# Optimization experiments

Measured on AMD Instinct MI355X. Metric: run time of the kernel, lower is better.

Reference implementation:

```python
import jax, jax.numpy as jnp
import numpy as np

N = 100000       # nodes
E = 1600000      # edges (before self loops)
D = 128          # emb_dim
L = 5            # num_layer
NBOND = 62       # num_bond_type
NNODE = 2159     # num_node_type + 2
BN_EPS = 1e-5


def setup_inputs() -> dict:
    key = jax.random.key(0)
    ks = jax.random.split(key, 8)
    x = jax.random.randint(ks[0], (N, 1), 0, NNODE)
    edge_index = jax.random.randint(ks[1], (2, E), 0, N)
    edge_attr = jax.random.randint(ks[2], (E, 1), 0, NBOND)
    x_emb = jax.random.normal(ks[3], (NNODE, D), dtype=jnp.float32) * 0.02
    lin_w = jax.random.normal(ks[4], (L, D, D), dtype=jnp.float32) * (1.0 / np.sqrt(D))
    lin_b = jnp.zeros((L, D), jnp.float32)
    edge_tab = jax.random.normal(ks[5], (L, NBOND, D), dtype=jnp.float32) * 0.02
    bn_gamma = jnp.ones((L, D), jnp.float32)
    bn_beta = jnp.zeros((L, D), jnp.float32)
    return {"x": x, "edge_index": edge_index, "edge_attr": edge_attr,
            "x_emb": x_emb, "lin_w": lin_w, "lin_b": lin_b,
            "edge_tab": edge_tab, "bn_gamma": bn_gamma, "bn_beta": bn_beta}


def reference(x, edge_index, edge_attr, x_emb, lin_w, lin_b, edge_tab, bn_gamma, bn_beta):
    # node embedding lookup: x_embedding(x[:, 0])
    h = x_emb[x[:, 0]]                                  # [N, D]

    # add self loops (same for every layer in the torch code)
    loop = jnp.arange(N)
    src = jnp.concatenate([edge_index[0], loop])        # [E+N] = j (source)
    dst = jnp.concatenate([edge_index[1], loop])        # [E+N] = i (target)
    eids = jnp.concatenate([edge_attr[:, 0], jnp.zeros((N,), edge_attr.dtype)])

    # GCN symmetric norm: deg from row (=src), deg_inv_sqrt[row]*deg_inv_sqrt[col]
    deg = jax.ops.segment_sum(jnp.ones(src.shape, h.dtype), src, num_segments=N)
    dinv = jnp.where(deg > 0, jax.lax.rsqrt(deg), jnp.zeros_like(deg))
    norm = (dinv[src] * dinv[dst])[:, None]             # [E+N, 1]

    for l in range(L):
        # linear transform of nodes
        hl = h @ lin_w[l].T + lin_b[l]                  # [N, D]
        # message: norm * (x_j + edge_embedding), gather from source nodes
        msg = norm * (hl[src] + edge_tab[l][eids])      # [E+N, D]
        # aggr='add': scatter_add into target nodes
        agg = jax.ops.segment_sum(msg, dst, num_segments=N)  # [N, D]
        # BatchNorm1d (training-mode batch statistics, biased variance)
        mean = agg.mean(axis=0)
        var = jnp.mean((agg - mean) ** 2, axis=0)
        h = (agg - mean) * jax.lax.rsqrt(var + BN_EPS) * bn_gamma[l] + bn_beta[l]
        if l < L - 1:
            h = jax.nn.relu(h)
        # dropout with drop_ratio=0 is identity
    # JK == 'last'
    return h
```

## Files before the change

### kernel.cpp

```cpp
#include <hip/hip_runtime.h>

#define NN 100000
#define NE 1600000
#define NT (NE + NN)
#define DD 128
#define NL 5
#define NB 62
#define BN_EPS 1e-5f
#define NBUCK 391
#define PSUMNB 6250

typedef unsigned short ushort_t;
typedef unsigned int uint_t;
typedef short bf8 __attribute__((ext_vector_type(8)));
typedef float f32x4 __attribute__((ext_vector_type(4)));

static __device__ __forceinline__ float4 ld4(const float* p) { return *(const float4*)p; }

static __device__ __forceinline__ float bfhi(uint_t u) {
    uint_t x = u & 0xFFFF0000u;
    return __builtin_bit_cast(float, x);
}
static __device__ __forceinline__ float bflo(uint_t u) {
    uint_t x = u << 16;
    return __builtin_bit_cast(float, x);
}
static __device__ __forceinline__ ushort_t f2bf(float f) {
    uint_t u = __builtin_bit_cast(uint_t, f);
    u += 0x7FFFu + ((u >> 16) & 1u);
    return (ushort_t)(u >> 16);
}


__global__ void k_init(int* gbh_d, int* gbh_s, float* scale, float* shift,
                       int* row_ptr) {
    int i = blockIdx.x * 256 + threadIdx.x;
    if (i < NBUCK) { gbh_d[i] = 0; gbh_s[i] = 0; }
    if (i < DD) { scale[i] = 1.f; shift[i] = 0.f; }
    if (i == 0) row_ptr[NN] = NT;
}

__global__ void k_cvt(const float* __restrict__ src, ushort_t* __restrict__ dst,
                      int total) {
    int i = blockIdx.x * 256 + threadIdx.x;
    if (i < total) dst[i] = f2bf(src[i]);
}

__global__ __launch_bounds__(256) void k_binhist(const int* __restrict__ ei,
                                                 int* __restrict__ gbh_d,
                                                 int* __restrict__ gbh_s) {
    __shared__ int hd[NBUCK], hs[NBUCK];
    int tid = threadIdx.x;
    for (int b = tid; b < NBUCK; b += 256) { hd[b] = 0; hs[b] = 0; }
    __syncthreads();
    for (int idx = blockIdx.x * 256 + tid; idx < NT; idx += gridDim.x * 256) {
        int d = (idx < NE) ? ei[NE + idx] : idx - NE;
        atomicAdd(&hd[d >> 8], 1);
        if (idx < NE) atomicAdd(&hs[ei[idx] >> 8], 1);
    }
    __syncthreads();
    for (int b = tid; b < NBUCK; b += 256) {
        if (hd[b]) atomicAdd(&gbh_d[b], hd[b]);
        if (hs[b]) atomicAdd(&gbh_s[b], hs[b]);
    }
}

__global__ void k_scan391(const int* __restrict__ gbh_d, const int* __restrict__ gbh_s,
                          int* __restrict__ bb_d, int* __restrict__ cur_d,
                          int* __restrict__ bb_s, int* __restrict__ cur_s) {
    __shared__ int s[512];
    const int* g = blockIdx.x ? gbh_s : gbh_d;
    int* bb = blockIdx.x ? bb_s : bb_d;
    int* cur = blockIdx.x ? cur_s : cur_d;
    int t = threadIdx.x;
    int v = (t < NBUCK) ? g[t] : 0;
    s[t] = v;
    __syncthreads();
    for (int off = 1; off < 512; off <<= 1) {
        int val = (t >= off) ? s[t - off] : 0;
        __syncthreads();
        s[t] += val;
        __syncthreads();
    }
    if (t < NBUCK) { int e = s[t] - v; bb[t] = e; cur[t] = e; }
    if (t == 511) bb[NBUCK] = s[511];
}

#define CHUNK 4096
__global__ __launch_bounds__(256) void k_scat_dst(const int* __restrict__ ei,
                                                  const int* __restrict__ ea,
                                                  int* __restrict__ gcur,
                                                  uint_t* __restrict__ rec) {
    __shared__ int lh[NBUCK];
    __shared__ int lbase[NBUCK];
    int tid = threadIdx.x;
    for (int b = tid; b < NBUCK; b += 256) lh[b] = 0;
    __syncthreads();
    int base = blockIdx.x * CHUNK;
    uint_t r[16];
    int bk[16];
#pragma unroll
    for (int k = 0; k < 16; ++k) {
        int idx = base + tid + k * 256;
        bk[k] = -1;
        if (idx < NT) {
            int s, d, eid;
            if (idx < NE) { s = ei[idx]; d = ei[NE + idx]; eid = ea[idx]; }
            else          { s = d = idx - NE; eid = 0; }
            bk[k] = d >> 8;
            r[k] = (uint_t)s | ((uint_t)eid << 17) | ((uint_t)(d & 255) << 24);
            atomicAdd(&lh[bk[k]], 1);
        }
    }
    __syncthreads();
    for (int b = tid; b < NBUCK; b += 256)
        if (lh[b]) lbase[b] = atomicAdd(&gcur[b], lh[b]);
    __syncthreads();
    for (int b = tid; b < NBUCK; b += 256) lh[b] = 0;
    __syncthreads();
#pragma unroll
    for (int k = 0; k < 16; ++k) {
        if (bk[k] >= 0) {
            int rk = atomicAdd(&lh[bk[k]], 1);
            rec[lbase[bk[k]] + rk] = r[k];
        }
    }
}

__global__ __launch_bounds__(256) void k_scat_src(const int* __restrict__ ei,
                                                  int* __restrict__ gcur,
                                                  int* __restrict__ rec) {
    __shared__ int lh[NBUCK];
    __shared__ int lbase[NBUCK];
    int tid = threadIdx.x;
    for (int b = tid; b < NBUCK; b += 256) lh[b] = 0;
    __syncthreads();
    int base = blockIdx.x * CHUNK;
    int r[16];
    int bk[16];
#pragma unroll
    for (int k = 0; k < 16; ++k) {
        int idx = base + tid + k * 256;
        bk[k] = -1;
        if (idx < NE) {
            r[k] = ei[idx];
            bk[k] = r[k] >> 8;
            atomicAdd(&lh[bk[k]], 1);
        }
    }
    __syncthreads();
    for (int b = tid; b < NBUCK; b += 256)
        if (lh[b]) lbase[b] = atomicAdd(&gcur[b], lh[b]);
    __syncthreads();
    for (int b = tid; b < NBUCK; b += 256) lh[b] = 0;
    __syncthreads();
#pragma unroll
    for (int k = 0; k < 16; ++k) {
        if (bk[k] >= 0) {
            int rk = atomicAdd(&lh[bk[k]], 1);
            rec[lbase[bk[k]] + rk] = r[k];
        }
    }
}

__global__ __launch_bounds__(256) void k_srcfin(const int* __restrict__ rec,
                                                const int* __restrict__ bb,
                                                float* __restrict__ dinv) {
    __shared__ int h[256];
    int tid = threadIdx.x;
    h[tid] = 0;
    __syncthreads();
    int lo = bb[blockIdx.x], hi = bb[blockIdx.x + 1];
    for (int i = lo + tid; i < hi; i += 256) atomicAdd(&h[rec[i] & 255], 1);
    __syncthreads();
    int v = blockIdx.x * 256 + tid;
    if (v < NN) dinv[v] = rsqrtf((float)(h[tid] + 1));
}

__global__ __launch_bounds__(256) void k_dstfin(const uint_t* __restrict__ rec,
                                                const int* __restrict__ bb,
                                                const float* __restrict__ dinv,
                                                int* __restrict__ row_ptr,
                                                int* __restrict__ s_pack,
                                                float* __restrict__ s_norm) {
    __shared__ int h[256], sc[256], rpE[256];
    int tid = threadIdx.x;
    h[tid] = 0;
    __syncthreads();
    int lo = bb[blockIdx.x], hi = bb[blockIdx.x + 1];
    for (int i = lo + tid; i < hi; i += 256) atomicAdd(&h[(rec[i] >> 24) & 255], 1);
    __syncthreads();
    sc[tid] = h[tid];
    __syncthreads();
    for (int off = 1; off < 256; off <<= 1) {
        int val = (tid >= off) ? sc[tid - off] : 0;
        __syncthreads();
        sc[tid] += val;
        __syncthreads();
    }
    rpE[tid] = sc[tid] - h[tid];
    int v = blockIdx.x * 256 + tid;
    if (v < NN) row_ptr[v] = lo + rpE[tid];
    h[tid] = 0;
    __syncthreads();
    for (int i = lo + tid; i < hi; i += 256) {
        uint_t u = rec[i];
        int dl = (u >> 24) & 255;
        int rk = atomicAdd(&h[dl], 1);
        int slot = lo + rpE[dl] + rk;
        int s = u & 0x1FFFF;
        int e = (u >> 17) & 0x3F;
        s_pack[slot] = s | (e << 20);
        s_norm[slot] = dinv[s] * dinv[(blockIdx.x << 8) + dl];
    }
}

__global__ void k_h0b(const int* __restrict__ x, const float* __restrict__ emb,
                      ushort_t* __restrict__ Xb, int n) {
    int v = blockIdx.x * 16 + (threadIdx.x >> 4);
    if (v >= n) return;
    int c8 = (threadIdx.x & 15) * 8;
    const float* src = &emb[x[v] * DD + c8];
    uint_t pk[4];
#pragma unroll
    for (int j = 0; j < 4; ++j)
        pk[j] = (uint_t)f2bf(src[2 * j]) | ((uint_t)f2bf(src[2 * j + 1]) << 16);
    *(uint4*)&Xb[(size_t)v * DD + c8] = make_uint4(pk[0], pk[1], pk[2], pk[3]);
}


__global__ __launch_bounds__(256, 2) void k_gemm(const ushort_t* __restrict__ Xb,
                                                 const ushort_t* __restrict__ Wb,
                                                 const float* __restrict__ bias,
                                                 const float* __restrict__ scale,
                                                 const float* __restrict__ shift,
                                                 ushort_t* __restrict__ C,
                                                 int n, int relu) {
    __shared__ ushort_t As[128 * DD];
    __shared__ ushort_t Bs[128 * DD];
    const int tid = threadIdx.x;
    const int r0 = blockIdx.x * 128;
    const int rl = tid >> 4;
    const int kg = tid & 15;

    float sc[8], sh[8];
    *(float4*)&sc[0] = ld4(&scale[kg * 8]);
    *(float4*)&sc[4] = ld4(&scale[kg * 8 + 4]);
    *(float4*)&sh[0] = ld4(&shift[kg * 8]);
    *(float4*)&sh[4] = ld4(&shift[kg * 8 + 4]);

#pragma unroll
    for (int it = 0; it < 8; ++it) {
        int row = rl + it * 16;
        int grow = r0 + row;
        uint4 v = make_uint4(0, 0, 0, 0);
        if (grow < n) v = *(const uint4*)&Xb[(size_t)grow * DD + kg * 8];
        uint_t pk[4];
        const uint_t* pv = (const uint_t*)&v;
#pragma unroll
        for (int j = 0; j < 4; ++j) {
            float lo = fmaf(bflo(pv[j]), sc[2 * j], sh[2 * j]);
            float hi = fmaf(bfhi(pv[j]), sc[2 * j + 1], sh[2 * j + 1]);
            if (relu) { lo = fmaxf(lo, 0.f); hi = fmaxf(hi, 0.f); }
            pk[j] = (uint_t)f2bf(lo) | ((uint_t)f2bf(hi) << 16);
        }
        *(uint4*)&As[row * DD + (kg ^ (row & 7)) * 8] = make_uint4(pk[0], pk[1], pk[2], pk[3]);
        uint4 wv = *(const uint4*)&Wb[row * DD + kg * 8];
        *(uint4*)&Bs[row * DD + (kg ^ (row & 7)) * 8] = wv;
    }
    __syncthreads();

    const int w = tid >> 6;
    const int lane = tid & 63;
    const int lr = lane & 15;
    const int lg = lane >> 4;

    f32x4 acc[2][8];
#pragma unroll
    for (int rf = 0; rf < 2; ++rf)
#pragma unroll
        for (int cf = 0; cf < 8; ++cf)
#pragma unroll
            for (int r = 0; r < 4; ++r) acc[rf][cf][r] = 0.f;

#pragma unroll
    for (int ks = 0; ks < 4; ++ks) {
        int kgg = ks * 4 + lg;
        bf8 a0, a1;
        {
            int row = w * 32 + lr;
            a0 = *(bf8*)&As[row * DD + (kgg ^ (row & 7)) * 8];
            row += 16;
            a1 = *(bf8*)&As[row * DD + (kgg ^ (row & 7)) * 8];
        }
#pragma unroll
        for (int cf = 0; cf < 8; ++cf) {
            int col = cf * 16 + lr;
            bf8 b = *(bf8*)&Bs[col * DD + (kgg ^ (col & 7)) * 8];
            acc[0][cf] = __builtin_amdgcn_mfma_f32_16x16x32_bf16(a0, b, acc[0][cf], 0, 0, 0);
            acc[1][cf] = __builtin_amdgcn_mfma_f32_16x16x32_bf16(a1, b, acc[1][cf], 0, 0, 0);
        }
    }

#pragma unroll
    for (int cf = 0; cf < 8; ++cf) {
        int col = cf * 16 + lr;
        float bi = bias[col];
#pragma unroll
        for (int rf = 0; rf < 2; ++rf) {
#pragma unroll
            for (int r = 0; r < 4; ++r) {
                int grow = r0 + w * 32 + rf * 16 + lg * 4 + r;
                if (grow < n) C[(size_t)grow * DD + col] = f2bf(acc[rf][cf][r] + bi);
            }
        }
    }
}

__global__ __launch_bounds__(256) void k_agg(const ushort_t* __restrict__ hl,
                                             const ushort_t* __restrict__ etab,
                                             const int* __restrict__ row_ptr,
                                             const int* __restrict__ s_pack,
                                             const float* __restrict__ s_norm,
                                             ushort_t* __restrict__ aggb,
                                             float* __restrict__ psumA,
                                             float* __restrict__ psumB, int n) {
    __shared__ float lsA[4][DD], lsB[4][DD];
    int tid = threadIdx.x;

    int v = blockIdx.x * 16 + (tid >> 4);
    int lane8 = (tid & 15) * 8;
    int p0 = row_ptr[v], p1 = row_ptr[v + 1];
    float acc[8];
#pragma unroll
    for (int j = 0; j < 8; ++j) acc[j] = 0.f;
    for (int p = p0; p < p1; ++p) {
        int c = s_pack[p];
        float nr = s_norm[p];
        int s = c & 0xFFFFF;
        int e = c >> 20;
        uint4 hv = *(const uint4*)&hl[s * DD + lane8];
        uint4 ev = *(const uint4*)&etab[e * DD + lane8];
        acc[0] = fmaf(nr, bflo(hv.x) + bflo(ev.x), acc[0]);
        acc[1] = fmaf(nr, bfhi(hv.x) + bfhi(ev.x), acc[1]);
        acc[2] = fmaf(nr, bflo(hv.y) + bflo(ev.y), acc[2]);
        acc[3] = fmaf(nr, bfhi(hv.y) + bfhi(ev.y), acc[3]);
        acc[4] = fmaf(nr, bflo(hv.z) + bflo(ev.z), acc[4]);
        acc[5] = fmaf(nr, bfhi(hv.z) + bfhi(ev.z), acc[5]);
        acc[6] = fmaf(nr, bflo(hv.w) + bflo(ev.w), acc[6]);
        acc[7] = fmaf(nr, bfhi(hv.w) + bfhi(ev.w), acc[7]);
    }
    uint_t pk[4];
#pragma unroll
    for (int j = 0; j < 4; ++j)
        pk[j] = (uint_t)f2bf(acc[2 * j]) | ((uint_t)f2bf(acc[2 * j + 1]) << 16);
    *(uint4*)&aggb[(size_t)v * DD + lane8] = make_uint4(pk[0], pk[1], pk[2], pk[3]);

    float s0[8], s1[8];
#pragma unroll
    for (int j = 0; j < 8; ++j) { s0[j] = acc[j]; s1[j] = acc[j] * acc[j]; }
#pragma unroll
    for (int m = 16; m <= 32; m <<= 1) {
#pragma unroll
        for (int j = 0; j < 8; ++j) {
            s0[j] += __shfl_xor(s0[j], m);
            s1[j] += __shfl_xor(s1[j], m);
        }
    }
    int wv = tid >> 6;
    int lane = tid & 63;
    if (lane < 16) {
#pragma unroll
        for (int j = 0; j < 8; ++j) {
            lsA[wv][lane8 + j] = s0[j];
            lsB[wv][lane8 + j] = s1[j];
        }
    }
    __syncthreads();
    if (tid < DD) {
        psumA[(size_t)blockIdx.x * DD + tid] =
            lsA[0][tid] + lsA[1][tid] + lsA[2][tid] + lsA[3][tid];
        psumB[(size_t)blockIdx.x * DD + tid] =
            lsB[0][tid] + lsB[1][tid] + lsB[2][tid] + lsB[3][tid];
    }
}

__global__ __launch_bounds__(256) void k_bnfinal2(const float* __restrict__ psumA,
                                                  const float* __restrict__ psumB,
                                                  const float* __restrict__ gamma,
                                                  const float* __restrict__ beta,
                                                  float* __restrict__ scale,
                                                  float* __restrict__ shift, int n) {
    __shared__ float rs[256], rss[256];
    int d = blockIdx.x;
    int t = threadIdx.x;
    float s = 0.f, ss = 0.f;
    for (int i = t; i < PSUMNB; i += 256) {
        s += psumA[(size_t)i * DD + d];
        ss += psumB[(size_t)i * DD + d];
    }
    rs[t] = s; rss[t] = ss;
    __syncthreads();
    for (int off = 128; off > 0; off >>= 1) {
        if (t < off) { rs[t] += rs[t + off]; rss[t] += rss[t + off]; }
        __syncthreads();
    }
    if (t == 0) {
        float mean = rs[0] / (float)n;
        float var = rss[0] / (float)n - mean * mean;
        float sc = gamma[d] * rsqrtf(var + BN_EPS);
        scale[d] = sc;
        shift[d] = beta[d] - mean * sc;
    }
}

__global__ void k_bnapply(const ushort_t* __restrict__ Xb, float* __restrict__ out,
                          const float* __restrict__ scale,
                          const float* __restrict__ shift, int total8) {
    int i = blockIdx.x * blockDim.x + threadIdx.x;
    int stride = gridDim.x * blockDim.x;
    for (; i < total8; i += stride) {
        int c8 = (i & 15) * 8;
        uint4 v = *(const uint4*)&Xb[(size_t)i * 8];
        float4 sc0 = ld4(&scale[c8]), sc1 = ld4(&scale[c8 + 4]);
        float4 sh0 = ld4(&shift[c8]), sh1 = ld4(&shift[c8 + 4]);
        float4 o0, o1;
        o0.x = fmaf(bflo(v.x), sc0.x, sh0.x);
        o0.y = fmaf(bfhi(v.x), sc0.y, sh0.y);
        o0.z = fmaf(bflo(v.y), sc0.z, sh0.z);
        o0.w = fmaf(bfhi(v.y), sc0.w, sh0.w);
        o1.x = fmaf(bflo(v.z), sc1.x, sh1.x);
        o1.y = fmaf(bfhi(v.z), sc1.y, sh1.y);
        o1.z = fmaf(bflo(v.w), sc1.z, sh1.z);
        o1.w = fmaf(bfhi(v.w), sc1.w, sh1.w);
        *(float4*)&out[(size_t)i * 8] = o0;
        *(float4*)&out[(size_t)i * 8 + 4] = o1;
    }
}


extern "C" void kernel_launch(void* const* d_in, const int* in_sizes, int n_in,
                              void* d_out, int out_size, void* d_ws, size_t ws_size,
                              hipStream_t stream) {
    const int* x        = (const int*)d_in[0];
    const int* ei       = (const int*)d_in[1];
    const int* ea       = (const int*)d_in[2];
    const float* x_emb  = (const float*)d_in[3];
    const float* lin_w  = (const float*)d_in[4];
    const float* lin_b  = (const float*)d_in[5];
    const float* etab   = (const float*)d_in[6];
    const float* gamma  = (const float*)d_in[7];
    const float* beta   = (const float*)d_in[8];
    float* OUT = (float*)d_out;

    char* w = (char*)d_ws;
    size_t off = 0;
    auto alloc = [&](size_t bytes) -> void* {
        off = (off + 255) & ~(size_t)255;
        void* p = w + off;
        off += bytes;
        return p;
    };
    ushort_t* Xb     = (ushort_t*)alloc((size_t)NN * DD * 2);
    ushort_t* hl     = (ushort_t*)alloc((size_t)NN * DD * 2);
    ushort_t* etabb  = (ushort_t*)alloc((size_t)NL * NB * DD * 2);
    ushort_t* Wb     = (ushort_t*)alloc((size_t)NL * DD * DD * 2);
    uint_t* rec_d    = (uint_t*)alloc((size_t)NT * 4);
    int*    rec_s    = (int*)alloc((size_t)NE * 4);
    int*   s_pack    = (int*)alloc((size_t)NT * 4);
    float* s_norm    = (float*)alloc((size_t)NT * 4);
    int*   rowp      = (int*)alloc((size_t)(NN + 1) * 4);
    float* dinv      = (float*)alloc((size_t)NN * 4);
    int*   gbh_d     = (int*)alloc((size_t)NBUCK * 4);
    int*   gbh_s     = (int*)alloc((size_t)NBUCK * 4);
    int*   bb_d      = (int*)alloc((size_t)(NBUCK + 1) * 4);
    int*   bb_s      = (int*)alloc((size_t)(NBUCK + 1) * 4);
    int*   cur_d     = (int*)alloc((size_t)NBUCK * 4);
    int*   cur_s     = (int*)alloc((size_t)NBUCK * 4);
    float* psumA     = (float*)alloc((size_t)DD * PSUMNB * 4);
    float* psumB     = (float*)alloc((size_t)DD * PSUMNB * 4);
    float* scale     = (float*)alloc((size_t)DD * 4);
    float* shift     = (float*)alloc((size_t)DD * 4);

    const int etabTot = NL * NB * DD;
    const int wTot = NL * DD * DD;

    k_init<<<(NN + 255) / 256, 256, 0, stream>>>(gbh_d, gbh_s, scale, shift, rowp);
    k_cvt<<<(etabTot + 255) / 256, 256, 0, stream>>>(etab, etabb, etabTot);
    k_cvt<<<(wTot + 255) / 256, 256, 0, stream>>>(lin_w, Wb, wTot);
    k_binhist<<<256, 256, 0, stream>>>(ei, gbh_d, gbh_s);
    k_scan391<<<2, 512, 0, stream>>>(gbh_d, gbh_s, bb_d, cur_d, bb_s, cur_s);
    k_scat_dst<<<(NT + CHUNK - 1) / CHUNK, 256, 0, stream>>>(ei, ea, cur_d, rec_d);
    k_scat_src<<<(NE + CHUNK - 1) / CHUNK, 256, 0, stream>>>(ei, cur_s, rec_s);
    k_srcfin<<<NBUCK, 256, 0, stream>>>(rec_s, bb_s, dinv);
    k_dstfin<<<NBUCK, 256, 0, stream>>>(rec_d, bb_d, dinv, rowp, s_pack, s_norm);
    k_h0b<<<(NN + 15) / 16, 256, 0, stream>>>(x, x_emb, Xb, NN);

    for (int l = 0; l < NL; ++l) {
        k_gemm<<<(NN + 127) / 128, 256, 0, stream>>>(Xb, Wb + (size_t)l * DD * DD,
                                                     lin_b + (size_t)l * DD,
                                                     scale, shift, hl, NN, l > 0 ? 1 : 0);
        k_agg<<<PSUMNB, 256, 0, stream>>>(hl, etabb + (size_t)l * NB * DD,
                                          rowp, s_pack, s_norm, Xb, psumA, psumB, NN);
        k_bnfinal2<<<DD, 256, 0, stream>>>(psumA, psumB, gamma + (size_t)l * DD,
                                           beta + (size_t)l * DD, scale, shift, NN);
    }
    k_bnapply<<<(NN * DD / 8 + 255) / 256, 256, 0, stream>>>(Xb, OUT, scale, shift,
                                                             NN * DD / 8);
}
```

Measured before the change: 793.5 us.

## Split each node's edge loop across a wavefront, fuse scatter kernels, two-stage BN reduce

The aggregation kernel now gives each destination node a full 64-lane wavefront: four 16-lane groups take interleaved edges and combine their partial sums with cross-lane shuffles. This is meant to expose more memory-level parallelism for the random row gathers. Blocks grow to 1024 threads, which raises shared-memory use and per-block sync cost. The separate dst and src bucket-scatter passes are merged into one kernel that reads edge_index once. The column-strided BN statistics reduction is replaced by a coalesced two-stage reduction (128 partial blocks, then one final block).

```diff
diff --git a/kernel.cpp b/kernel.cpp
--- a/kernel.cpp
+++ b/kernel.cpp
@@ -9,6 +9,7 @@
 #define BN_EPS 1e-5f
 #define NBUCK 391
 #define PSUMNB 6250
+#define RED1 128
 
 typedef unsigned short ushort_t;
 typedef unsigned int uint_t;
@@ -87,78 +88,54 @@
 }
 
 #define CHUNK 4096
-__global__ __launch_bounds__(256) void k_scat_dst(const int* __restrict__ ei,
-                                                  const int* __restrict__ ea,
-                                                  int* __restrict__ gcur,
-                                                  uint_t* __restrict__ rec) {
-    __shared__ int lh[NBUCK];
-    __shared__ int lbase[NBUCK];
+__global__ __launch_bounds__(256) void k_scat2(const int* __restrict__ ei,
+                                               const int* __restrict__ ea,
+                                               int* __restrict__ cur_d,
+                                               int* __restrict__ cur_s,
+                                               uint_t* __restrict__ rec_d,
+                                               int* __restrict__ rec_s) {
+    __shared__ int lhd[NBUCK], lbd[NBUCK], lhs[NBUCK], lbs[NBUCK];
     int tid = threadIdx.x;
-    for (int b = tid; b < NBUCK; b += 256) lh[b] = 0;
+    for (int b = tid; b < NBUCK; b += 256) { lhd[b] = 0; lhs[b] = 0; }
     __syncthreads();
     int base = blockIdx.x * CHUNK;
-    uint_t r[16];
-    int bk[16];
+    uint_t rd[16];
+    int rs[16], bkd[16], bks[16];
 #pragma unroll
     for (int k = 0; k < 16; ++k) {
         int idx = base + tid + k * 256;
-        bk[k] = -1;
+        bkd[k] = -1; bks[k] = -1;
         if (idx < NT) {
             int s, d, eid;
-            if (idx < NE) { s = ei[idx]; d = ei[NE + idx]; eid = ea[idx]; }
-            else          { s = d = idx - NE; eid = 0; }
-            bk[k] = d >> 8;
-            r[k] = (uint_t)s | ((uint_t)eid << 17) | ((uint_t)(d & 255) << 24);
-            atomicAdd(&lh[bk[k]], 1);
-        }
-    }
-    __syncthreads();
-    for (int b = tid; b < NBUCK; b += 256)
-        if (lh[b]) lbase[b] = atomicAdd(&gcur[b], lh[b]);
-    __syncthreads();
-    for (int b = tid; b < NBUCK; b += 256) lh[b] = 0;
+            if (idx < NE) {
+                s = ei[idx]; d = ei[NE + idx]; eid = ea[idx];
+                bks[k] = s >> 8; rs[k] = s;
+                atomicAdd(&lhs[bks[k]], 1);
+            } else {
+                s = d = idx - NE; eid = 0;
+            }
+            bkd[k] = d >> 8;
+            rd[k] = (uint_t)s | ((uint_t)eid << 17) | ((uint_t)(d & 255) << 24);
+            atomicAdd(&lhd[bkd[k]], 1);
+        }
+    }
+    __syncthreads();
+    for (int b = tid; b < NBUCK; b += 256) {
+        if (lhd[b]) lbd[b] = atomicAdd(&cur_d[b], lhd[b]);
+        if (lhs[b]) lbs[b] = atomicAdd(&cur_s[b], lhs[b]);
+    }
+    __syncthreads();
+    for (int b = tid; b < NBUCK; b += 256) { lhd[b] = 0; lhs[b] = 0; }
     __syncthreads();
 #pragma unroll
     for (int k = 0; k < 16; ++k) {
-        if (bk[k] >= 0) {
-            int rk = atomicAdd(&lh[bk[k]], 1);
-            rec[lbase[bk[k]] + rk] = r[k];
-        }
-    }
-}
-
-__global__ __launch_bounds__(256) void k_scat_src(const int* __restrict__ ei,
-                                                  int* __restrict__ gcur,
-                                                  int* __restrict__ rec) {
-    __shared__ int lh[NBUCK];
-    __shared__ int lbase[NBUCK];
-    int tid = threadIdx.x;
-    for (int b = tid; b < NBUCK; b += 256) lh[b] = 0;
-    __syncthreads();
-    int base = blockIdx.x * CHUNK;
-    int r[16];
-    int bk[16];
-#pragma unroll
-    for (int k = 0; k < 16; ++k) {
-        int idx = base + tid + k * 256;
-        bk[k] = -1;
-        if (idx < NE) {
-            r[k] = ei[idx];
-            bk[k] = r[k] >> 8;
-            atomicAdd(&lh[bk[k]], 1);
-        }
-    }
-    __syncthreads();
-    for (int b = tid; b < NBUCK; b += 256)
-        if (lh[b]) lbase[b] = atomicAdd(&gcur[b], lh[b]);
-    __syncthreads();
-    for (int b = tid; b < NBUCK; b += 256) lh[b] = 0;
-    __syncthreads();
-#pragma unroll
-    for (int k = 0; k < 16; ++k) {
-        if (bk[k] >= 0) {
-            int rk = atomicAdd(&lh[bk[k]], 1);
-            rec[lbase[bk[k]] + rk] = r[k];
+        if (bkd[k] >= 0) {
+            int rk = atomicAdd(&lhd[bkd[k]], 1);
+            rec_d[lbd[bkd[k]] + rk] = rd[k];
+        }
+        if (bks[k] >= 0) {
+            int rk = atomicAdd(&lhs[bks[k]], 1);
+            rec_s[lbs[bks[k]] + rk] = rs[k];
         }
     }
 }
@@ -317,29 +294,33 @@
     }
 }
 
-__global__ __launch_bounds__(256) void k_agg(const ushort_t* __restrict__ hl,
-                                             const ushort_t* __restrict__ etab,
-                                             const int* __restrict__ row_ptr,
-                                             const int* __restrict__ s_pack,
-                                             const float* __restrict__ s_norm,
-                                             ushort_t* __restrict__ aggb,
-                                             float* __restrict__ psumA,
-                                             float* __restrict__ psumB, int n) {
-    __shared__ float lsA[4][DD], lsB[4][DD];
+__global__ __launch_bounds__(1024) void k_agg(const ushort_t* __restrict__ hl,
+                                              const ushort_t* __restrict__ etab,
+                                              const int* __restrict__ row_ptr,
+                                              const int* __restrict__ s_pack,
+                                              const float* __restrict__ s_norm,
+                                              ushort_t* __restrict__ aggb,
+                                              float* __restrict__ psumA,
+                                              float* __restrict__ psumB, int n) {
+    __shared__ float lsA[16][DD], lsB[16][DD];
     int tid = threadIdx.x;
-
-    int v = blockIdx.x * 16 + (tid >> 4);
-    int lane8 = (tid & 15) * 8;
+    int wv = tid >> 6;
+    int lane = tid & 63;
+    int g = lane >> 4;
+    int fl = lane & 15;
+    int lane8 = fl * 8;
+    int v = blockIdx.x * 16 + wv;
     int p0 = row_ptr[v], p1 = row_ptr[v + 1];
+
     float acc[8];
 #pragma unroll
     for (int j = 0; j < 8; ++j) acc[j] = 0.f;
-    for (int p = p0; p < p1; ++p) {
+    for (int p = p0 + g; p < p1; p += 4) {
         int c = s_pack[p];
         float nr = s_norm[p];
         int s = c & 0xFFFFF;
         int e = c >> 20;
-        uint4 hv = *(const uint4*)&hl[s * DD + lane8];
+        uint4 hv = *(const uint4*)&hl[(size_t)s * DD + lane8];
         uint4 ev = *(const uint4*)&etab[e * DD + lane8];
         acc[0] = fmaf(nr, bflo(hv.x) + bflo(ev.x), acc[0]);
         acc[1] = fmaf(nr, bfhi(hv.x) + bfhi(ev.x), acc[1]);
@@ -350,64 +331,75 @@
         acc[6] = fmaf(nr, bflo(hv.w) + bflo(ev.w), acc[6]);
         acc[7] = fmaf(nr, bfhi(hv.w) + bfhi(ev.w), acc[7]);
     }
-    uint_t pk[4];
-#pragma unroll
-    for (int j = 0; j < 4; ++j)
-        pk[j] = (uint_t)f2bf(acc[2 * j]) | ((uint_t)f2bf(acc[2 * j + 1]) << 16);
-    *(uint4*)&aggb[(size_t)v * DD + lane8] = make_uint4(pk[0], pk[1], pk[2], pk[3]);
-
-    float s0[8], s1[8];
-#pragma unroll
-    for (int j = 0; j < 8; ++j) { s0[j] = acc[j]; s1[j] = acc[j] * acc[j]; }
-#pragma unroll
-    for (int m = 16; m <= 32; m <<= 1) {
+#pragma unroll
+    for (int j = 0; j < 8; ++j) {
+        acc[j] += __shfl_xor(acc[j], 16);
+        acc[j] += __shfl_xor(acc[j], 32);
+    }
+    if (g == 0) {
+        uint_t pk[4];
+#pragma unroll
+        for (int j = 0; j < 4; ++j)
+            pk[j] = (uint_t)f2bf(acc[2 * j]) | ((uint_t)f2bf(acc[2 * j + 1]) << 16);
+        *(uint4*)&aggb[(size_t)v * DD + lane8] = make_uint4(pk[0], pk[1], pk[2], pk[3]);
 #pragma unroll
         for (int j = 0; j < 8; ++j) {
-            s0[j] += __shfl_xor(s0[j], m);
-            s1[j] += __shfl_xor(s1[j], m);
-        }
-    }
-    int wv = tid >> 6;
-    int lane = tid & 63;
-    if (lane < 16) {
-#pragma unroll
-        for (int j = 0; j < 8; ++j) {
-            lsA[wv][lane8 + j] = s0[j];
-            lsB[wv][lane8 + j] = s1[j];
+            lsA[wv][lane8 + j] = acc[j];
+            lsB[wv][lane8 + j] = acc[j] * acc[j];
         }
     }
     __syncthreads();
     if (tid < DD) {
-        psumA[(size_t)blockIdx.x * DD + tid] =
-            lsA[0][tid] + lsA[1][tid] + lsA[2][tid] + lsA[3][tid];
-        psumB[(size_t)blockIdx.x * DD + tid] =
-            lsB[0][tid] + lsB[1][tid] + lsB[2][tid] + lsB[3][tid];
-    }
-}
-
-__global__ __launch_bounds__(256) void k_bnfinal2(const float* __restrict__ psumA,
-                                                  const float* __restrict__ psumB,
-                                                  const float* __restrict__ gamma,
-                                                  const float* __restrict__ beta,
-                                                  float* __restrict__ scale,
-                                                  float* __restrict__ shift, int n) {
-    __shared__ float rs[256], rss[256];
-    int d = blockIdx.x;
-    int t = threadIdx.x;
-    float s = 0.f, ss = 0.f;
-    for (int i = t; i < PSUMNB; i += 256) {
-        s += psumA[(size_t)i * DD + d];
-        ss += psumB[(size_t)i * DD + d];
-    }
-    rs[t] = s; rss[t] = ss;
-    __syncthreads();
-    for (int off = 128; off > 0; off >>= 1) {
-        if (t < off) { rs[t] += rs[t + off]; rss[t] += rss[t + off]; }
-        __syncthreads();
-    }
-    if (t == 0) {
-        float mean = rs[0] / (float)n;
-        float var = rss[0] / (float)n - mean * mean;
+        float a = 0.f, b = 0.f;
+#pragma unroll
+        for (int k = 0; k < 16; ++k) { a += lsA[k][tid]; b += lsB[k][tid]; }
+        psumA[(size_t)blockIdx.x * DD + tid] = a;
+        psumB[(size_t)blockIdx.x * DD + tid] = b;
+    }
+}
+
+__global__ __launch_bounds__(256) void k_bnred(const float* __restrict__ psumA,
+                                               const float* __restrict__ psumB,
+                                               float* __restrict__ partA,
+                                               float* __restrict__ partB) {
+    __shared__ float sa[2][DD], sb[2][DD];
+    int d = threadIdx.x & 127;
+    int half = threadIdx.x >> 7;
+    float a = 0.f, b = 0.f;
+    int iend = min(blockIdx.x * 49 + 49, PSUMNB);
+    for (int i = blockIdx.x * 49 + half; i < iend; i += 2) {
+        a += psumA[(size_t)i * DD + d];
+        b += psumB[(size_t)i * DD + d];
+    }
+    sa[half][d] = a; sb[half][d] = b;
+    __syncthreads();
+    if (threadIdx.x < DD) {
+        partA[blockIdx.x * DD + d] = sa[0][d] + sa[1][d];
+        partB[blockIdx.x * DD + d] = sb[0][d] + sb[1][d];
+    }
+}
+
+__global__ __launch_bounds__(256) void k_bnfin(const float* __restrict__ partA,
+                                               const float* __restrict__ partB,
+                                               const float* __restrict__ gamma,
+                                               const float* __restrict__ beta,
+                                               float* __restrict__ scale,
+                                               float* __restrict__ shift, int n) {
+    __shared__ float sa[2][DD], sb[2][DD];
+    int d = threadIdx.x & 127;
+    int half = threadIdx.x >> 7;
+    float a = 0.f, b = 0.f;
+    for (int i = half; i < RED1; i += 2) {
+        a += partA[i * DD + d];
+        b += partB[i * DD + d];
+    }
+    sa[half][d] = a; sb[half][d] = b;
+    __syncthreads();
+    if (threadIdx.x < DD) {
+        float s = sa[0][d] + sa[1][d];
+        float ss = sb[0][d] + sb[1][d];
+        float mean = s / (float)n;
+        float var = ss / (float)n - mean * mean;
         float sc = gamma[d] * rsqrtf(var + BN_EPS);
         scale[d] = sc;
         shift[d] = beta[d] - mean * sc;
@@ -479,6 +471,8 @@
     int*   cur_s     = (int*)alloc((size_t)NBUCK * 4);
     float* psumA     = (float*)alloc((size_t)DD * PSUMNB * 4);
     float* psumB     = (float*)alloc((size_t)DD * PSUMNB * 4);
+    float* partA     = (float*)alloc((size_t)DD * RED1 * 4);
+    float* partB     = (float*)alloc((size_t)DD * RED1 * 4);
     float* scale     = (float*)alloc((size_t)DD * 4);
     float* shift     = (float*)alloc((size_t)DD * 4);
 
@@ -490,8 +484,8 @@
     k_cvt<<<(wTot + 255) / 256, 256, 0, stream>>>(lin_w, Wb, wTot);
     k_binhist<<<256, 256, 0, stream>>>(ei, gbh_d, gbh_s);
     k_scan391<<<2, 512, 0, stream>>>(gbh_d, gbh_s, bb_d, cur_d, bb_s, cur_s);
-    k_scat_dst<<<(NT + CHUNK - 1) / CHUNK, 256, 0, stream>>>(ei, ea, cur_d, rec_d);
-    k_scat_src<<<(NE + CHUNK - 1) / CHUNK, 256, 0, stream>>>(ei, cur_s, rec_s);
+    k_scat2<<<(NT + CHUNK - 1) / CHUNK, 256, 0, stream>>>(ei, ea, cur_d, cur_s,
+                                                          rec_d, rec_s);
     k_srcfin<<<NBUCK, 256, 0, stream>>>(rec_s, bb_s, dinv);
     k_dstfin<<<NBUCK, 256, 0, stream>>>(rec_d, bb_d, dinv, rowp, s_pack, s_norm);
     k_h0b<<<(NN + 15) / 16, 256, 0, stream>>>(x, x_emb, Xb, NN);
@@ -500,10 +494,11 @@
         k_gemm<<<(NN + 127) / 128, 256, 0, stream>>>(Xb, Wb + (size_t)l * DD * DD,
                                                      lin_b + (size_t)l * DD,
                                                      scale, shift, hl, NN, l > 0 ? 1 : 0);
-        k_agg<<<PSUMNB, 256, 0, stream>>>(hl, etabb + (size_t)l * NB * DD,
-                                          rowp, s_pack, s_norm, Xb, psumA, psumB, NN);
-        k_bnfinal2<<<DD, 256, 0, stream>>>(psumA, psumB, gamma + (size_t)l * DD,
-                                           beta + (size_t)l * DD, scale, shift, NN);
+        k_agg<<<PSUMNB, 1024, 0, stream>>>(hl, etabb + (size_t)l * NB * DD,
+                                           rowp, s_pack, s_norm, Xb, psumA, psumB, NN);
+        k_bnred<<<RED1, 256, 0, stream>>>(psumA, psumB, partA, partB);
+        k_bnfin<<<1, 256, 0, stream>>>(partA, partB, gamma + (size_t)l * DD,
+                                       beta + (size_t)l * DD, scale, shift, NN);
     }
     k_bnapply<<<(NN * DD / 8 + 255) / 256, 256, 0, stream>>>(Xb, OUT, scale, shift,
                                                              NN * DD / 8);
```

Result: slower. 816.1 us (+2.8%).
